# Performance work log

Hardware: AMD Instinct MI355X
Metric: run time of the kernel (lower is better)

The kernel has to match this reference:

```python
import jax, jax.numpy as jnp
import numpy as np

LIGAND_W = 1.0
SIDECHAIN_W = 0.5
LIGAND_DIST_W = 0.2
SIDECHAIN_DIST_W = 0.1
CUTOFF = 5.0
EPS = 1e-12


def _pdist(x):
    # x: [..., N, 3] -> (dist [..., N, N], sq [..., N, N]); safe sqrt for grads
    d = x[..., :, None, :] - x[..., None, :, :]
    sq = jnp.sum(d * d, axis=-1)
    return jnp.sqrt(jnp.maximum(sq, EPS)), sq


def _masked_dist_loss(pred, tgt, valid):
    # pred/tgt: [..., N, 3], valid: [..., N] float. Returns (per-group loss, has-any flag)
    pd, _ = _pdist(pred)
    td, tsq = _pdist(tgt)
    pair = valid[..., :, None] * valid[..., None, :]
    dmask = pair * (tsq > 0.0).astype(pred.dtype) * (td <= CUTOFF).astype(pred.dtype)
    num = jnp.sum(dmask * (pd - td) ** 2, axis=(-1, -2))
    den = jnp.sum(dmask, axis=(-1, -2))
    return num / jnp.maximum(den, 1.0), den > 0.0


def setup_inputs() -> dict:
    key = jax.random.key(0)
    k1, k2, k3, k4, k5, k6 = jax.random.split(key, 6)
    B, L, R, A = 64, 512, 1024, 14
    ligand_tgt = jax.random.normal(k2, (B, L, 3), dtype=jnp.float32) * 3.0
    ligand_pred = ligand_tgt + 0.5 * jax.random.normal(k1, (B, L, 3), dtype=jnp.float32)
    sidechain_tgt = jax.random.normal(k4, (B, R, A, 3), dtype=jnp.float32) * 2.0
    sidechain_pred = sidechain_tgt + 0.5 * jax.random.normal(k3, (B, R, A, 3), dtype=jnp.float32)
    ligand_mask = jax.random.bernoulli(k5, 0.9, (B, L))
    atom_mask = jax.random.bernoulli(k6, 0.7, (B, R, A))
    return {
        'ligand_pred': ligand_pred, 'ligand_tgt': ligand_tgt,
        'sidechain_pred': sidechain_pred, 'sidechain_tgt': sidechain_tgt,
        'ligand_mask': ligand_mask, 'atom_mask': atom_mask,
    }


def reference(ligand_pred, ligand_tgt, sidechain_pred, sidechain_tgt, ligand_mask, atom_mask):
    f = ligand_pred.dtype
    lm = ligand_mask.astype(f)              # [B, L]
    am = atom_mask.astype(f)                # [B, R, A]

    # --- ligand coord loss: per-batch mse (mean over valid atoms * 3), then mean over batches ---
    se = jnp.sum((ligand_pred - ligand_tgt) ** 2, axis=-1) * lm   # [B, L]
    lig_cnt = jnp.sum(lm, axis=-1)                                # [B]
    ligand_loss = jnp.mean(jnp.sum(se, axis=-1) / (3.0 * jnp.maximum(lig_cnt, 1.0)))

    # --- ligand distance-preservation loss ---
    lig_d, lig_has = _masked_dist_loss(ligand_pred, ligand_tgt, lm)  # [B], [B]
    ligand_dist_loss = jnp.sum(jnp.where(lig_has, lig_d, 0.0)) / jnp.maximum(jnp.sum(lig_has.astype(f)), 1.0)

    # --- sidechain coord loss: per-atom mse (mean over 3), mean over all valid atoms ---
    atom_mse = jnp.mean((sidechain_pred - sidechain_tgt) ** 2, axis=-1)  # [B, R, A]
    sc_cnt = jnp.sum(am)
    sidechain_loss = jnp.sum(atom_mse * am) / jnp.maximum(sc_cnt, 1.0)

    # --- sidechain distance-preservation loss: per-residue groups ---
    sc_d, sc_has = _masked_dist_loss(sidechain_pred, sidechain_tgt, am)  # [B, R]
    sidechain_dist_loss = jnp.sum(jnp.where(sc_has, sc_d, 0.0)) / jnp.maximum(jnp.sum(sc_has.astype(f)), 1.0)

    total = (LIGAND_W * ligand_loss
             + LIGAND_DIST_W * ligand_dist_loss
             + SIDECHAIN_W * sidechain_loss
             + SIDECHAIN_DIST_W * sidechain_dist_loss)
    return total
```

## Files before the change

kernel.cpp:

```cpp
#include <hip/hip_runtime.h>

#define CUTOFF 5.0f
#define DEPS 1e-12f
#define FSQRT(x) __builtin_amdgcn_sqrtf(x)


#define GRID 1024

__global__ __launch_bounds__(256) void fused_kernel(
    const float* __restrict__ lig_pred, const float* __restrict__ lig_tgt,
    const int* __restrict__ lig_mask,
    const float* __restrict__ sc_pred, const float* __restrict__ sc_tgt,
    const int* __restrict__ sc_mask,
    float* __restrict__ ws) {
  const int tid = threadIdx.x;
  __shared__ float4 stage4[1344];
  __shared__ float red[4][4];

  if ((blockIdx.x & 1) == 0) {
    const int sb = blockIdx.x >> 1;
    float ax[7], ay[7], az[7];
    float bx[7], by[7], bz[7];
    float m[7];

    const float4* srcp = (const float4*)(sc_pred + (size_t)sb * 5376);
    for (int k = tid; k < 1344; k += 256) stage4[k] = srcp[k];
    __syncthreads();
    {
      const float* s = ((const float*)stage4) + tid * 21;
#pragma unroll
      for (int a = 0; a < 7; a++) { ax[a] = s[3 * a]; ay[a] = s[3 * a + 1]; az[a] = s[3 * a + 2]; }
    }
    __syncthreads();
    const float4* srct = (const float4*)(sc_tgt + (size_t)sb * 5376);
    for (int k = tid; k < 1344; k += 256) stage4[k] = srct[k];
    __syncthreads();
    {
      const float* s = ((const float*)stage4) + tid * 21;
#pragma unroll
      for (int a = 0; a < 7; a++) { bx[a] = s[3 * a]; by[a] = s[3 * a + 1]; bz[a] = s[3 * a + 2]; }
    }
    const int* mp = sc_mask + (size_t)sb * 1792 + tid * 7;
#pragma unroll
    for (int a = 0; a < 7; a++) m[a] = (mp[a] != 0) ? 1.f : 0.f;

    float mse = 0.f, am = 0.f;
#pragma unroll
    for (int a = 0; a < 7; a++) {
      float dx = ax[a] - bx[a], dy = ay[a] - by[a], dz = az[a] - bz[a];
      mse += m[a] * ((dx * dx + dy * dy + dz * dz) * (1.f / 3.f));
      am += m[a];
    }

    float num = 0.f, den = 0.f;
#pragma unroll
    for (int js = 0; js < 7; js++) {
#pragma unroll
      for (int side = 0; side < 2; side++) {
        float jx, jy, jz, kx, ky, kz, mj;
        if (side == 0) {
          jx = ax[js]; jy = ay[js]; jz = az[js];
          kx = bx[js]; ky = by[js]; kz = bz[js];
          mj = m[js];
        } else {
          jx = __shfl_xor(ax[js], 1, 64); jy = __shfl_xor(ay[js], 1, 64);
          jz = __shfl_xor(az[js], 1, 64);
          kx = __shfl_xor(bx[js], 1, 64); ky = __shfl_xor(by[js], 1, 64);
          kz = __shfl_xor(bz[js], 1, 64);
          mj = __shfl_xor(m[js], 1, 64);
        }
#pragma unroll
        for (int i = 0; i < 7; i++) {
          float dx = bx[i] - kx, dy = by[i] - ky, dz = bz[i] - kz;
          float tsq = dx * dx + dy * dy + dz * dz;
          float td = FSQRT(fmaxf(tsq, DEPS));
          float w = m[i] * mj;
          w = (tsq > 0.f) ? w : 0.f;
          w = (td <= CUTOFF) ? w : 0.f;
          float qx = ax[i] - jx, qy = ay[i] - jy, qz = az[i] - jz;
          float pd = FSQRT(fmaxf(qx * qx + qy * qy + qz * qz, DEPS));
          float d = pd - td;
          num += w * d * d;
          den += w;
        }
      }
    }
    float num_g = num + __shfl_xor(num, 1, 64);
    float den_g = den + __shfl_xor(den, 1, 64);
    float val = (den_g > 0.f) ? 0.5f * (num_g / fmaxf(den_g, 1.f)) : 0.f;
    float has = (den_g > 0.f) ? 0.5f : 0.f;

    for (int off = 32; off > 0; off >>= 1) {
      mse += __shfl_down(mse, off, 64);
      am += __shfl_down(am, off, 64);
      val += __shfl_down(val, off, 64);
      has += __shfl_down(has, off, 64);
    }
    int lane = tid & 63, wv = tid >> 6;
    if (lane == 0) { red[0][wv] = mse; red[1][wv] = am; red[2][wv] = val; red[3][wv] = has; }
    __syncthreads();
    if (tid == 0) {
      float* p = ws + 1088 + (size_t)sb * 4;
      p[0] = red[0][0] + red[0][1] + red[0][2] + red[0][3];
      p[1] = red[1][0] + red[1][1] + red[1][2] + red[1][3];
      p[2] = red[2][0] + red[2][1] + red[2][2] + red[2][3];
      p[3] = red[3][0] + red[3][1] + red[3][2] + red[3][3];
    }
  } else {
    const int L = 512;
    const int lb = blockIdx.x >> 1;
    const int b = lb >> 3;
    const int tile = lb & 7;
    const int i0 = tile * 64;
    const float* pb = lig_pred + (size_t)b * L * 3;
    const float* tb = lig_tgt + (size_t)b * L * 3;
    const int* mb = lig_mask + (size_t)b * L;

    float4* st4 = stage4;
    float4* sp4 = stage4 + 64;

    if (tid < 64) {
      int i = i0 + tid;
      st4[tid] = make_float4(tb[3 * i], tb[3 * i + 1], tb[3 * i + 2], (mb[i] != 0) ? 1.f : 0.f);
    } else if (tid < 128) {
      int i = i0 + tid - 64;
      sp4[tid - 64] = make_float4(pb[3 * i], pb[3 * i + 1], pb[3 * i + 2], 0.f);
    }
    __syncthreads();

    float num = 0.f, den = 0.f, se = 0.f, cnt = 0.f;
#pragma unroll
    for (int k = 0; k < 2; k++) {
      const int js = i0 + k * 256 + tid;
      if (js < L) {
        float pjx = pb[3 * js], pjy = pb[3 * js + 1], pjz = pb[3 * js + 2];
        float tjx = tb[3 * js], tjy = tb[3 * js + 1], tjz = tb[3 * js + 2];
        float mj = (mb[js] != 0) ? 1.f : 0.f;
        if (tile == 0) {
          float dx = pjx - tjx, dy = pjy - tjy, dz = pjz - tjz;
          se += mj * (dx * dx + dy * dy + dz * dz);
          cnt += mj;
        }
#pragma unroll 4
        for (int ii = 0; ii < 64; ii++) {
          float4 ti = st4[ii];
          float4 pi = sp4[ii];
          float w = (js > i0 + ii) ? ti.w * mj : 0.f;
          float dx = ti.x - tjx, dy = ti.y - tjy, dz = ti.z - tjz;
          float tsq = dx * dx + dy * dy + dz * dz;
          float td = FSQRT(fmaxf(tsq, DEPS));
          w = (tsq > 0.f) ? w : 0.f;
          w = (td <= CUTOFF) ? w : 0.f;
          float qx = pi.x - pjx, qy = pi.y - pjy, qz = pi.z - pjz;
          float pd = FSQRT(fmaxf(qx * qx + qy * qy + qz * qz, DEPS));
          float d = pd - td;
          num += w * d * d;
          den += w;
        }
      }
    }

    for (int off = 32; off > 0; off >>= 1) {
      num += __shfl_down(num, off, 64);
      den += __shfl_down(den, off, 64);
      se += __shfl_down(se, off, 64);
      cnt += __shfl_down(cnt, off, 64);
    }
    int lane = tid & 63, wv = tid >> 6;
    if (lane == 0) { red[0][wv] = num; red[1][wv] = den; red[2][wv] = se; red[3][wv] = cnt; }
    __syncthreads();
    if (tid == 0) {
      ws[lb * 2 + 0] = red[0][0] + red[0][1] + red[0][2] + red[0][3];
      ws[lb * 2 + 1] = red[1][0] + red[1][1] + red[1][2] + red[1][3];
      if (tile == 0) {
        float se_t = red[2][0] + red[2][1] + red[2][2] + red[2][3];
        float cnt_t = red[3][0] + red[3][1] + red[3][2] + red[3][3];
        ws[1024 + b] = se_t / (3.f * fmaxf(cnt_t, 1.f));
      }
    }
  }
}

__global__ __launch_bounds__(256) void finalize_kernel(const float* __restrict__ ws,
                                                       float* __restrict__ out) {
  const int tid = threadIdx.x;
  __shared__ float sred[4][4];

  const float* sc = ws + 1088;
  float s0 = 0.f, s1 = 0.f, s2 = 0.f, s3 = 0.f;
  for (int i = tid; i < 512; i += 256) {
    s0 += sc[4 * i + 0]; s1 += sc[4 * i + 1]; s2 += sc[4 * i + 2]; s3 += sc[4 * i + 3];
  }
  for (int off = 32; off > 0; off >>= 1) {
    s0 += __shfl_down(s0, off, 64);
    s1 += __shfl_down(s1, off, 64);
    s2 += __shfl_down(s2, off, 64);
    s3 += __shfl_down(s3, off, 64);
  }
  int lane = tid & 63, wv = tid >> 6;
  if (lane == 0) { sred[0][wv] = s0; sred[1][wv] = s1; sred[2][wv] = s2; sred[3][wv] = s3; }
  __syncthreads();

  float lval = 0.f, lhas = 0.f, lcoord = 0.f;
  if (tid < 64) {
    float n = 0.f, d = 0.f;
    for (int t = 0; t < 8; t++) {
      n += ws[(tid * 8 + t) * 2 + 0];
      d += ws[(tid * 8 + t) * 2 + 1];
    }
    lval = (d > 0.f) ? n / fmaxf(d, 1.f) : 0.f;
    lhas = (d > 0.f) ? 1.f : 0.f;
    lcoord = ws[1024 + tid];
    for (int off = 32; off > 0; off >>= 1) {
      lval += __shfl_down(lval, off, 64);
      lhas += __shfl_down(lhas, off, 64);
      lcoord += __shfl_down(lcoord, off, 64);
    }
  }
  if (tid == 0) {
    float sc_mse = sred[0][0] + sred[0][1] + sred[0][2] + sred[0][3];
    float sc_am = sred[1][0] + sred[1][1] + sred[1][2] + sred[1][3];
    float sc_val = sred[2][0] + sred[2][1] + sred[2][2] + sred[2][3];
    float sc_has = sred[3][0] + sred[3][1] + sred[3][2] + sred[3][3];
    float ligand_loss = lcoord * (1.f / 64.f);
    float ligand_dist_loss = lval / fmaxf(lhas, 1.f);
    float sidechain_loss = sc_mse / fmaxf(sc_am, 1.f);
    float sidechain_dist_loss = sc_val / fmaxf(sc_has, 1.f);
    out[0] = ligand_loss + 0.2f * ligand_dist_loss + 0.5f * sidechain_loss +
             0.1f * sidechain_dist_loss;
  }
}

extern "C" void kernel_launch(void* const* d_in, const int* in_sizes, int n_in,
                              void* d_out, int out_size, void* d_ws, size_t ws_size,
                              hipStream_t stream) {
  const float* ligand_pred = (const float*)d_in[0];
  const float* ligand_tgt = (const float*)d_in[1];
  const float* sidechain_pred = (const float*)d_in[2];
  const float* sidechain_tgt = (const float*)d_in[3];
  const int* ligand_mask = (const int*)d_in[4];
  const int* atom_mask = (const int*)d_in[5];
  float* out = (float*)d_out;
  float* ws = (float*)d_ws;

  fused_kernel<<<GRID, 256, 0, stream>>>(ligand_pred, ligand_tgt, ligand_mask,
                                         sidechain_pred, sidechain_tgt, atom_mask, ws);
  finalize_kernel<<<1, 256, 0, stream>>>(ws, out);
}
```

Baseline: 109.9 us.

## Balance ligand triangle tiles by pairing row chunks and reorder block assignment

Each ligand block now takes two 32-row chunks from opposite ends of the triangular pair matrix (t and 15-t), so every block does about the same amount of pair work instead of the first tiles doing far more than the last. Sidechain blocks now take the first 512 block IDs and ligand blocks the rest, replacing the even/odd interleave. The inner loop splits its accumulation into two partial sums to shorten the dependency chain. The cost is an extra loop pass and a more complex staging step, and the new block order changes which work runs concurrently on the device.

```diff
diff --git a/kernel.cpp b/kernel.cpp
--- a/kernel.cpp
+++ b/kernel.cpp
@@ -5,7 +5,9 @@
 #define FSQRT(x) __builtin_amdgcn_sqrtf(x)
 
 
-#define GRID 1024
+#define NSC_BLK 512
+#define NLIG_BLK 512
+#define GRID (NSC_BLK + NLIG_BLK)
 
 __global__ __launch_bounds__(256) void fused_kernel(
     const float* __restrict__ lig_pred, const float* __restrict__ lig_tgt,
@@ -17,8 +19,8 @@
   __shared__ float4 stage4[1344];
   __shared__ float red[4][4];
 
-  if ((blockIdx.x & 1) == 0) {
-    const int sb = blockIdx.x >> 1;
+  if (blockIdx.x < NSC_BLK) {
+    const int sb = blockIdx.x;
     float ax[7], ay[7], az[7];
     float bx[7], by[7], bz[7];
     float m[7];
@@ -108,10 +110,11 @@
     }
   } else {
     const int L = 512;
-    const int lb = blockIdx.x >> 1;
+    const int lb = blockIdx.x - NSC_BLK;
     const int b = lb >> 3;
-    const int tile = lb & 7;
-    const int i0 = tile * 64;
+    const int t = lb & 7;
+    const int i0a = 32 * t;
+    const int i0b = 32 * (15 - t);
     const float* pb = lig_pred + (size_t)b * L * 3;
     const float* tb = lig_tgt + (size_t)b * L * 3;
     const int* mb = lig_mask + (size_t)b * L;
@@ -119,33 +122,39 @@
     float4* st4 = stage4;
     float4* sp4 = stage4 + 64;
 
-    if (tid < 64) {
-      int i = i0 + tid;
-      st4[tid] = make_float4(tb[3 * i], tb[3 * i + 1], tb[3 * i + 2], (mb[i] != 0) ? 1.f : 0.f);
-    } else if (tid < 128) {
-      int i = i0 + tid - 64;
-      sp4[tid - 64] = make_float4(pb[3 * i], pb[3 * i + 1], pb[3 * i + 2], 0.f);
-    }
-    __syncthreads();
-
-    float num = 0.f, den = 0.f, se = 0.f, cnt = 0.f;
+    if (tid < 128) {
+      int which = tid >> 5;
+      int idx = tid & 31;
+      int i = ((which & 1) ? i0b : i0a) + idx;
+      if (which < 2) {
+        st4[(which << 5) + idx] =
+            make_float4(tb[3 * i], tb[3 * i + 1], tb[3 * i + 2], (mb[i] != 0) ? 1.f : 0.f);
+      } else {
+        sp4[((which & 1) << 5) + idx] =
+            make_float4(pb[3 * i], pb[3 * i + 1], pb[3 * i + 2], 0.f);
+      }
+    }
+    __syncthreads();
+
+    float num0 = 0.f, den0 = 0.f, num1 = 0.f, den1 = 0.f, se = 0.f, cnt = 0.f;
+
 #pragma unroll
     for (int k = 0; k < 2; k++) {
-      const int js = i0 + k * 256 + tid;
+      const int js = i0a + (k << 8) + tid;
       if (js < L) {
         float pjx = pb[3 * js], pjy = pb[3 * js + 1], pjz = pb[3 * js + 2];
         float tjx = tb[3 * js], tjy = tb[3 * js + 1], tjz = tb[3 * js + 2];
         float mj = (mb[js] != 0) ? 1.f : 0.f;
-        if (tile == 0) {
+        if (t == 0) {
           float dx = pjx - tjx, dy = pjy - tjy, dz = pjz - tjz;
           se += mj * (dx * dx + dy * dy + dz * dz);
           cnt += mj;
         }
 #pragma unroll 4
-        for (int ii = 0; ii < 64; ii++) {
+        for (int ii = 0; ii < 32; ii++) {
           float4 ti = st4[ii];
           float4 pi = sp4[ii];
-          float w = (js > i0 + ii) ? ti.w * mj : 0.f;
+          float w = (js > i0a + ii) ? ti.w * mj : 0.f;
           float dx = ti.x - tjx, dy = ti.y - tjy, dz = ti.z - tjz;
           float tsq = dx * dx + dy * dy + dz * dz;
           float td = FSQRT(fmaxf(tsq, DEPS));
@@ -154,12 +163,38 @@
           float qx = pi.x - pjx, qy = pi.y - pjy, qz = pi.z - pjz;
           float pd = FSQRT(fmaxf(qx * qx + qy * qy + qz * qz, DEPS));
           float d = pd - td;
-          num += w * d * d;
-          den += w;
-        }
-      }
-    }
-
+          if (ii & 1) { num1 += w * d * d; den1 += w; }
+          else        { num0 += w * d * d; den0 += w; }
+        }
+      }
+    }
+
+    {
+      const int js = i0b + tid;
+      if (js < L) {
+        float pjx = pb[3 * js], pjy = pb[3 * js + 1], pjz = pb[3 * js + 2];
+        float tjx = tb[3 * js], tjy = tb[3 * js + 1], tjz = tb[3 * js + 2];
+        float mj = (mb[js] != 0) ? 1.f : 0.f;
+#pragma unroll 4
+        for (int ii = 0; ii < 32; ii++) {
+          float4 ti = st4[32 + ii];
+          float4 pi = sp4[32 + ii];
+          float w = (js > i0b + ii) ? ti.w * mj : 0.f;
+          float dx = ti.x - tjx, dy = ti.y - tjy, dz = ti.z - tjz;
+          float tsq = dx * dx + dy * dy + dz * dz;
+          float td = FSQRT(fmaxf(tsq, DEPS));
+          w = (tsq > 0.f) ? w : 0.f;
+          w = (td <= CUTOFF) ? w : 0.f;
+          float qx = pi.x - pjx, qy = pi.y - pjy, qz = pi.z - pjz;
+          float pd = FSQRT(fmaxf(qx * qx + qy * qy + qz * qz, DEPS));
+          float d = pd - td;
+          if (ii & 1) { num1 += w * d * d; den1 += w; }
+          else        { num0 += w * d * d; den0 += w; }
+        }
+      }
+    }
+
+    float num = num0 + num1, den = den0 + den1;
     for (int off = 32; off > 0; off >>= 1) {
       num += __shfl_down(num, off, 64);
       den += __shfl_down(den, off, 64);
@@ -172,7 +207,7 @@
     if (tid == 0) {
       ws[lb * 2 + 0] = red[0][0] + red[0][1] + red[0][2] + red[0][3];
       ws[lb * 2 + 1] = red[1][0] + red[1][1] + red[1][2] + red[1][3];
-      if (tile == 0) {
+      if (t == 0) {
         float se_t = red[2][0] + red[2][1] + red[2][2] + red[2][3];
         float cnt_t = red[3][0] + red[3][1] + red[3][2] + red[3][3];
         ws[1024 + b] = se_t / (3.f * fmaxf(cnt_t, 1.f));
```

New measurement: 105.7 us. 1.04x faster.
